# Performance work log

Hardware: AMD Instinct MI355X
Metric: run time of the kernel (lower is better)

## Reference

```python
import jax, jax.numpy as jnp
import numpy as np

HIDDEN = 256
BATCH = 8
N_A = 2048
N_B = 2048


def setup_inputs() -> dict:
    key = jax.random.key(0)
    ks = jax.random.split(key, 9)
    s = 1.0 / np.sqrt(HIDDEN)  # torch Linear default init scale
    return {
        "A": jax.random.normal(ks[0], (BATCH, N_A, HIDDEN), dtype=jnp.float32),
        "B": jax.random.normal(ks[1], (BATCH, N_B, HIDDEN), dtype=jnp.float32),
        "mask_B": jax.random.randint(ks[2], (BATCH, N_B), 0, 2, dtype=jnp.int32),
        "Wq": jax.random.uniform(ks[3], (HIDDEN, HIDDEN), jnp.float32, -s, s),
        "bq": jax.random.uniform(ks[4], (HIDDEN,), jnp.float32, -s, s),
        "Wk": jax.random.uniform(ks[5], (HIDDEN, HIDDEN), jnp.float32, -s, s),
        "bk": jax.random.uniform(ks[6], (HIDDEN,), jnp.float32, -s, s),
        "Wv": jax.random.uniform(ks[7], (HIDDEN, HIDDEN), jnp.float32, -s, s),
        "bv": jax.random.uniform(ks[8], (HIDDEN,), jnp.float32, -s, s),
    }


def reference(A, B, mask_B, Wq, bq, Wk, bk, Wv, bv):
    # QKV projections (torch Linear: x @ W.T + b)
    Q = A @ Wq.T + bq          # [B, N_A, H]
    K = B @ Wk.T + bk          # [B, N_B, H]
    V = B @ Wv.T + bv          # [B, N_B, H]
    scale = 1.0 / jnp.sqrt(jnp.asarray(Q.shape[-1], Q.dtype))
    scores = jnp.einsum("bnh,bmh->bnm", Q, K) * scale  # [B, N_A, N_B]
    neg_inf = jnp.finfo(scores.dtype).min
    scores = jnp.where(mask_B[:, None, :] == 0, neg_inf, scores)
    attn = jax.nn.softmax(scores, axis=-1)
    out = jnp.einsum("bnm,bmh->bnh", attn, V)          # [B, N_A, H]
    return out
```

## Files before the change

kernel.cpp:

```cpp
#include <hip/hip_runtime.h>


typedef __attribute__((ext_vector_type(8))) __bf16 bf16x8;
typedef __attribute__((ext_vector_type(4))) __bf16 bf16x4;
typedef __attribute__((ext_vector_type(4))) float f32x4;

#if __has_builtin(__builtin_amdgcn_exp2f)
#define EXP2(x) __builtin_amdgcn_exp2f(x)
#else
#define EXP2(x) exp2f(x)
#endif

#define MFMA16(a, b, c) __builtin_amdgcn_mfma_f32_16x16x32_bf16((a), (b), (c), 0, 0, 0)

typedef const __attribute__((address_space(1))) char gas_char;
typedef __attribute__((address_space(3))) char las_char;

static __device__ __forceinline__ void gload16(const void* g, void* l) {
  __builtin_amdgcn_global_load_lds((gas_char*)g, (las_char*)l, 16, 0, 0);
}

static __device__ __forceinline__ bf16x8 pack8(f32x4 a, f32x4 b) {
  bf16x8 r;
  r[0] = (__bf16)a[0]; r[1] = (__bf16)a[1]; r[2] = (__bf16)a[2]; r[3] = (__bf16)a[3];
  r[4] = (__bf16)b[0]; r[5] = (__bf16)b[1]; r[6] = (__bf16)b[2]; r[7] = (__bf16)b[3];
  return r;
}

__global__ __launch_bounds__(256) void wprep_kernel(
    const float* __restrict__ Wq, const float* __restrict__ Wk,
    const float* __restrict__ Wv, const int* __restrict__ mask,
    __bf16* __restrict__ Wb, float* __restrict__ mb) {
  const int bid = blockIdx.x;
  if (bid < 96) {
    int c = bid * 256 + threadIdx.x;
    int w_id = c >> 13;
    int j = c & 8191;
    const float* __restrict__ W = (w_id == 0) ? Wq : (w_id == 1 ? Wk : Wv);
    int n = j >> 5;
    int c5 = j & 31;
    int qtr = c5 >> 3;
    int k8 = (c5 & 7) << 3;
    const float* wp = &W[n * 256 + qtr * 64 + k8];
    f32x4 w0 = *(const f32x4*)wp;
    f32x4 w1 = *(const f32x4*)(wp + 4);
    if (w_id == 0) {
      const float cs = 0.090168440f;
      w0[0] *= cs; w0[1] *= cs; w0[2] *= cs; w0[3] *= cs;
      w1[0] *= cs; w1[1] *= cs; w1[2] *= cs; w1[3] *= cs;
    }
    int kx = k8 ^ ((n & 7) << 3);
    *(bf16x8*)&Wb[(size_t)w_id * 65536 + qtr * 16384 + n * 64 + kx] =
        pack8(w0, w1);
  } else {
    int i = (bid - 96) * 256 + threadIdx.x;
    if (i < 8 * 2048) mb[i] = (mask[i] != 0) ? 0.0f : -1.0e30f;
  }
}

__global__ __launch_bounds__(256, 2) void proj_kernel(
    const float* __restrict__ A, const float* __restrict__ Bm,
    const __bf16* __restrict__ Wb,
    const float* __restrict__ bq, const float* __restrict__ bk,
    const float* __restrict__ bv,
    __bf16* __restrict__ QF, __bf16* __restrict__ KF, __bf16* __restrict__ VF) {
  extern __shared__ char smem[];
  const int pid = blockIdx.x;
  const bool isQ = (pid < 256);
  const int rb = (pid & 255) << 6;
  const float* __restrict__ X = isQ ? A : Bm;
  const int tid = threadIdx.x;
  const int w = tid >> 6, l = tid & 63, lo = l & 15, g = l >> 4;
  const int r0 = rb + w * 16;

  #define STAGEW(srcbase, buf)                                                \
    {                                                                         \
      const char* gw = (srcbase) + w * 1024 + l * 16;                         \
      char* lw = smem + (buf)*32768 + w * 1024;                               \
      gload16(gw, lw);                                                        \
      gload16(gw + 4096, lw + 4096);                                          \
      gload16(gw + 8192, lw + 8192);                                          \
      gload16(gw + 12288, lw + 12288);                                        \
      gload16(gw + 16384, lw + 16384);                                        \
      gload16(gw + 20480, lw + 20480);                                        \
      gload16(gw + 24576, lw + 24576);                                        \
      gload16(gw + 28672, lw + 28672);                                        \
    }

  const char* Wq_ = (const char*)Wb;
  const char* Wk_ = (const char*)(Wb + 65536);
  const char* Wv_ = (const char*)(Wb + 131072);

  if (isQ) {
    STAGEW(Wq_, 0);
  } else {
    STAGEW(Wk_, 0);
  }

  bf16x8 xf[8];
#pragma unroll
  for (int q8 = 0; q8 < 8; ++q8) {
    const float* xp = &X[(r0 + lo) * 256 + q8 * 32 + g * 8];
    xf[q8] = pack8(*(const f32x4*)xp, *(const f32x4*)(xp + 4));
  }
  __syncthreads();

  if (isQ) {
    f32x4 acc[16];
#pragma unroll
    for (int j = 0; j < 16; ++j) acc[j] = (f32x4){0.f, 0.f, 0.f, 0.f};
    for (int qtr = 0; qtr < 4; ++qtr) {
      const int cur = qtr & 1;
      if (qtr < 3) STAGEW(Wq_ + (qtr + 1) * 32768, cur ^ 1);
      const __bf16* Wl = (const __bf16*)(smem + cur * 32768);
#pragma unroll
      for (int ks2 = 0; ks2 < 2; ++ks2) {
        bf16x8 xcur = xf[qtr * 2 + ks2];
#pragma unroll
        for (int nt = 0; nt < 16; ++nt) {
          int n = nt * 16 + lo;
          int kchunk = (ks2 * 4 + g) ^ (n & 7);
          bf16x8 wf = *(const bf16x8*)&Wl[n * 64 + kchunk * 8];
          acc[nt] = MFMA16(xcur, wf, acc[nt]);
        }
      }
      __syncthreads();
    }
    const float cs = 0.090168440f;
    const size_t rgbase = (size_t)(r0 >> 4) << 12;
#pragma unroll
    for (int nt = 0; nt < 16; ++nt) {
      int h = nt * 16 + lo;
      float bb = bq[h] * cs;
      size_t hpart = (size_t)((h >> 5) << 9) + (((h >> 3) & 3) << 7) + (h & 7);
#pragma unroll
      for (int r = 0; r < 4; ++r) {
        int R = r0 + g * 4 + r;
        QF[rgbase + hpart + ((R & 15) << 3)] = (__bf16)(acc[nt][r] + bb);
      }
    }
  } else {
    f32x4 accK[16], accV[16];
#pragma unroll
    for (int j = 0; j < 16; ++j) {
      accK[j] = (f32x4){0.f, 0.f, 0.f, 0.f};
      accV[j] = (f32x4){0.f, 0.f, 0.f, 0.f};
    }
    for (int c = 0; c < 8; ++c) {
      const int cur = c & 1;
      if (c < 7) {
        const int cn = c + 1;
        const char* src = ((cn & 1) ? Wv_ : Wk_) + (cn >> 1) * 32768;
        STAGEW(src, cur ^ 1);
      }
      const __bf16* Wl = (const __bf16*)(smem + cur * 32768);
      const int qtr = c >> 1;
#pragma unroll
      for (int ks2 = 0; ks2 < 2; ++ks2) {
        bf16x8 xcur = xf[qtr * 2 + ks2];
#pragma unroll
        for (int nt = 0; nt < 16; ++nt) {
          int n = nt * 16 + lo;
          int kchunk = (ks2 * 4 + g) ^ (n & 7);
          bf16x8 wf = *(const bf16x8*)&Wl[n * 64 + kchunk * 8];
          if (c & 1) {
            accV[nt] = MFMA16(wf, xcur, accV[nt]);
          } else {
            accK[nt] = MFMA16(xcur, wf, accK[nt]);
          }
        }
      }
      __syncthreads();
    }
    const size_t rgbase = (size_t)(r0 >> 4) << 12;
#pragma unroll
    for (int nt = 0; nt < 16; ++nt) {
      int h = nt * 16 + lo;
      float bb = bk[h];
      size_t hpart = (size_t)((h >> 5) << 9) + (((h >> 3) & 3) << 7) + (h & 7);
#pragma unroll
      for (int r = 0; r < 4; ++r) {
        int R = r0 + g * 4 + r;
        KF[rgbase + hpart + ((R & 15) << 3)] = (__bf16)(accK[nt][r] + bb);
      }
    }
    const int bidx = r0 >> 11;
    const int nb = r0 & 2047;
    __bf16* __restrict__ Vo = VF + (size_t)bidx * 524288;
#pragma unroll
    for (int ht = 0; ht < 16; ++ht)
#pragma unroll
      for (int r = 0; r < 4; ++r) {
        int h = ht * 16 + g * 4 + r;
        int n = nb + lo;
        Vo[((size_t)(n >> 6) << 14) + ((h >> 4) << 10) + (((n >> 3) & 7) << 7) +
           ((h & 15) << 3) + (n & 7)] = (__bf16)(accV[ht][r] + bv[h]);
      }
  }
}

__global__ __launch_bounds__(256, 2) void attn_kernel(
    const __bf16* __restrict__ QF, const __bf16* __restrict__ KF,
    const __bf16* __restrict__ VF, const float* __restrict__ mb,
    __bf16* __restrict__ Opart, float* __restrict__ lpart,
    float* __restrict__ out, int chunk, int direct) {
  extern __shared__ char smem[];
  const int bid = blockIdx.x;
  const int b = bid & 7;
  const int rest = bid >> 3;
  const int qt = rest & 15;
  const int s = rest >> 4;
  const int tid = threadIdx.x;
  const int w = tid >> 6, l = tid & 63, lo = l & 15, g = l >> 4;
  const int q0 = qt * 128 + w * 32;
  const __bf16* __restrict__ Qb = QF + ((size_t)b * 2048 + q0) * 256;
  const __bf16* __restrict__ Kb = KF + (size_t)b * 2048 * 256;
  const __bf16* __restrict__ Vb = VF + (size_t)b * 524288;
  const float* __restrict__ mbb = mb + b * 2048;
  __bf16* Pw = (__bf16*)(smem + 65536) + w * 1280;
  float* mbl = (float*)(smem + 75776);

  bf16x8 qf[2][8];
#pragma unroll
  for (int u = 0; u < 2; ++u)
#pragma unroll
    for (int hs = 0; hs < 8; ++hs)
      qf[u][hs] = *(const bf16x8*)&Qb[u * 4096 + hs * 512 + l * 8];

  f32x4 oacc[2][16];
#pragma unroll
  for (int u = 0; u < 2; ++u)
#pragma unroll
    for (int i = 0; i < 16; ++i) oacc[u][i] = (f32x4){0.f, 0.f, 0.f, 0.f};
  float lsum[2] = {0.f, 0.f};

  const int kv0 = s * chunk;
  const int niter = chunk >> 5;

  #define STAGE_K(kvb, buf)                                                   \
    {                                                                         \
      const char* gk = (const char*)(Kb + (size_t)(kvb) * 256) + w * 4096 +   \
                       l * 16;                                                \
      char* lk = smem + (buf)*16384 + w * 4096;                               \
      gload16(gk, lk);                                                        \
      gload16(gk + 1024, lk + 1024);                                          \
      gload16(gk + 2048, lk + 2048);                                          \
      gload16(gk + 3072, lk + 3072);                                          \
    }
  #define STAGE_V(kvb, buf)                                                   \
    {                                                                         \
      const char* gv = (const char*)(Vb + (((size_t)(kvb) >> 6) << 14) +      \
                                     (((kvb) >> 5) & 1) * 512) +              \
                       w * 8192 + l * 16;                                     \
      char* lv = smem + 32768 + (buf)*16384 + w * 4096;                       \
      gload16(gv, lv);                                                        \
      gload16(gv + 2048, lv + 1024);                                          \
      gload16(gv + 4096, lv + 2048);                                          \
      gload16(gv + 6144, lv + 3072);                                          \
    }

  if (!direct)
    for (int j = tid; j < chunk; j += 256) mbl[j] = mbb[kv0 + j];
  STAGE_K(kv0, 0);
  STAGE_V(kv0, 0);
  __syncthreads();

  for (int it = 0; it < niter; ++it) {
    const int kvb = kv0 + (it << 5);
    const int cur = it & 1;
    const bool pre = (it + 1 < niter);
    if (pre) STAGE_K(kvb + 32, cur ^ 1);
    const char* kbase = smem + cur * 16384;
    const char* vbase = smem + 32768 + cur * 16384;

    f32x4 sacc[2][2];
#pragma unroll
    for (int u = 0; u < 2; ++u)
#pragma unroll
      for (int t = 0; t < 2; ++t) sacc[u][t] = (f32x4){0.f, 0.f, 0.f, 0.f};
    __builtin_amdgcn_s_setprio(1);
#pragma unroll
    for (int t = 0; t < 2; ++t)
#pragma unroll
      for (int hs = 0; hs < 8; ++hs) {
        bf16x8 kf = *(const bf16x8*)(kbase + t * 8192 + hs * 1024 + l * 16);
        sacc[0][t] = MFMA16(kf, qf[0][hs], sacc[0][t]);
        sacc[1][t] = MFMA16(kf, qf[1][hs], sacc[1][t]);
      }
    __builtin_amdgcn_s_setprio(0);

    f32x4 bias4[2];
#pragma unroll
    for (int t = 0; t < 2; ++t) {
      if (direct)
        bias4[t] = *(const f32x4*)&mbb[kvb + t * 16 + g * 4];
      else
        bias4[t] = *(const f32x4*)&mbl[(it << 5) + t * 16 + g * 4];
    }
#pragma unroll
    for (int u = 0; u < 2; ++u)
#pragma unroll
      for (int t = 0; t < 2; ++t) {
        float p0 = EXP2(sacc[u][t][0] + bias4[t][0]);
        float p1 = EXP2(sacc[u][t][1] + bias4[t][1]);
        float p2 = EXP2(sacc[u][t][2] + bias4[t][2]);
        float p3 = EXP2(sacc[u][t][3] + bias4[t][3]);
        lsum[u] += (p0 + p1) + (p2 + p3);
        bf16x4 pk;
        pk[0] = (__bf16)p0; pk[1] = (__bf16)p1;
        pk[2] = (__bf16)p2; pk[3] = (__bf16)p3;
        *(bf16x4*)&Pw[u * 640 + lo * 40 + t * 16 + g * 4] = pk;
      }
    bf16x8 pf[2];
#pragma unroll
    for (int u = 0; u < 2; ++u)
      pf[u] = *(const bf16x8*)&Pw[u * 640 + lo * 40 + g * 8];

    if (direct || !pre) {
      asm volatile("s_waitcnt vmcnt(0)" ::: "memory");
    } else {
      asm volatile("s_waitcnt vmcnt(4)" ::: "memory");
    }
    __builtin_amdgcn_s_barrier();
    __builtin_amdgcn_sched_barrier(0);

    if (pre) STAGE_V(kvb + 32, cur ^ 1);

    __builtin_amdgcn_s_setprio(1);
#pragma unroll
    for (int ht = 0; ht < 16; ++ht) {
      bf16x8 vf = *(const bf16x8*)(vbase + ht * 1024 + l * 16);
      oacc[0][ht] = MFMA16(vf, pf[0], oacc[0][ht]);
      oacc[1][ht] = MFMA16(vf, pf[1], oacc[1][ht]);
    }
    __builtin_amdgcn_s_setprio(0);

    if (direct || !pre) {
      asm volatile("s_waitcnt vmcnt(0)" ::: "memory");
    } else {
      asm volatile("s_waitcnt vmcnt(4)" ::: "memory");
    }
    __builtin_amdgcn_s_barrier();
    __builtin_amdgcn_sched_barrier(0);
  }

#pragma unroll
  for (int u = 0; u < 2; ++u) {
    float ls = lsum[u];
    ls += __shfl_xor(ls, 16);
    ls += __shfl_xor(ls, 32);
    const int q0u = q0 + u * 16;
    if (direct) {
      float inv = 1.0f / ls;
      float* __restrict__ Ob = out + ((size_t)b * 2048 + q0u) * 256;
#pragma unroll
      for (int ht = 0; ht < 16; ++ht) {
        f32x4 v = oacc[u][ht];
        v[0] *= inv; v[1] *= inv; v[2] *= inv; v[3] *= inv;
        *(f32x4*)&Ob[lo * 256 + ht * 16 + g * 4] = v;
      }
    } else {
      const size_t rowbase = (size_t)(s * 8 + b) * 2048 + q0u;
      __bf16* __restrict__ Ob = Opart + rowbase * 256;
#pragma unroll
      for (int ht = 0; ht < 16; ++ht) {
        f32x4 v = oacc[u][ht];
        bf16x4 pk;
        pk[0] = (__bf16)v[0]; pk[1] = (__bf16)v[1];
        pk[2] = (__bf16)v[2]; pk[3] = (__bf16)v[3];
        *(bf16x4*)&Ob[lo * 256 + ht * 16 + g * 4] = pk;
      }
      if (l < 16) lpart[rowbase + lo] = ls;
    }
  }
}

__global__ __launch_bounds__(256) void combine_kernel(
    const __bf16* __restrict__ Opart, const float* __restrict__ lpart,
    float* __restrict__ out, int nsplit) {
  int t = blockIdx.x * 256 + threadIdx.x;
  int row = t >> 6;
  int h4 = (t & 63) << 2;
  f32x4 acc = (f32x4){0.f, 0.f, 0.f, 0.f};
  float denom = 0.f;
  for (int s = 0; s < nsplit; ++s) {
    denom += lpart[s * 16384 + row];
    bf16x4 o = *(const bf16x4*)&Opart[((size_t)s * 16384 + row) * 256 + h4];
    acc[0] += (float)o[0]; acc[1] += (float)o[1];
    acc[2] += (float)o[2]; acc[3] += (float)o[3];
  }
  float inv = 1.0f / denom;
  f32x4 r;
  r[0] = acc[0] * inv; r[1] = acc[1] * inv;
  r[2] = acc[2] * inv; r[3] = acc[3] * inv;
  *(f32x4*)&out[(size_t)row * 256 + h4] = r;
}

extern "C" void kernel_launch(void* const* d_in, const int* in_sizes, int n_in,
                              void* d_out, int out_size, void* d_ws, size_t ws_size,
                              hipStream_t stream) {
  const float* A = (const float*)d_in[0];
  const float* B = (const float*)d_in[1];
  const int* mask = (const int*)d_in[2];
  const float* Wq = (const float*)d_in[3];
  const float* bq = (const float*)d_in[4];
  const float* Wk = (const float*)d_in[5];
  const float* bk = (const float*)d_in[6];
  const float* Wv = (const float*)d_in[7];
  const float* bv = (const float*)d_in[8];

  char* ws = (char*)d_ws;
  __bf16* QF = (__bf16*)(ws);
  __bf16* KF = (__bf16*)(ws + (8ull << 20));
  __bf16* VF = (__bf16*)(ws + (16ull << 20));
  float* mb = (float*)(ws + (24ull << 20));
  float* lpart = (float*)(ws + (24ull << 20) + 0x10000);
  __bf16* Wb = (__bf16*)(ws + (24ull << 20) + 0x90000);
  __bf16* Opart = (__bf16*)(ws + (25ull << 20));

  const size_t base = 25ull << 20;
  const size_t part = 8ull << 20;
  int S;
  if (ws_size >= base + 4 * part) S = 4;
  else if (ws_size >= base + 2 * part) S = 2;
  else if (ws_size >= base + 1 * part) S = 1;
  else S = 0;

  const int PSMEM = 65536;
  (void)hipFuncSetAttribute((const void*)proj_kernel,
                            hipFuncAttributeMaxDynamicSharedMemorySize, PSMEM);
  const int SMEM = 65536 + 4 * 1280 * 2 + 2048;
  (void)hipFuncSetAttribute((const void*)attn_kernel,
                            hipFuncAttributeMaxDynamicSharedMemorySize, SMEM);

  wprep_kernel<<<160, 256, 0, stream>>>(Wq, Wk, Wv, mask, Wb, mb);
  proj_kernel<<<512, 256, PSMEM, stream>>>(A, B, Wb, bq, bk, bv, QF, KF, VF);
  if (S == 0) {
    attn_kernel<<<128, 256, SMEM, stream>>>(QF, KF, VF, mb, nullptr, nullptr,
                                            (float*)d_out, 2048, 1);
  } else {
    attn_kernel<<<128 * S, 256, SMEM, stream>>>(QF, KF, VF, mb, Opart, lpart,
                                                nullptr, 2048 / S, 0);
    combine_kernel<<<4096, 256, 0, stream>>>(Opart, lpart, (float*)d_out, S);
  }
}
```

Before: 84.10 us.

## Switch attention loop to 64-wide KV tiles with single-buffered staged K/V

Each attention iteration now processes 64 keys instead of 32. K and V live in a single 32 KB buffer each rather than two double-buffered halves. The next K tile is loaded during the PV MFMAs and the next V tile during the following QK phase, which halves the number of loop iterations and barriers. The mask bias is now read from global memory instead of being staged in LDS. The trade-off is full vmcnt(0) waits and less overlap, since each load must complete before its single buffer is reused.

```diff
diff --git a/kernel.cpp b/kernel.cpp
--- a/kernel.cpp
+++ b/kernel.cpp
@@ -217,8 +217,7 @@
   const __bf16* __restrict__ Kb = KF + (size_t)b * 2048 * 256;
   const __bf16* __restrict__ Vb = VF + (size_t)b * 524288;
   const float* __restrict__ mbb = mb + b * 2048;
-  __bf16* Pw = (__bf16*)(smem + 65536) + w * 1280;
-  float* mbl = (float*)(smem + 75776);
+  __bf16* Pw = (__bf16*)(smem + 65536) + w * 1152;
 
   bf16x8 qf[2][8];
 #pragma unroll
@@ -235,113 +234,106 @@
   float lsum[2] = {0.f, 0.f};
 
   const int kv0 = s * chunk;
-  const int niter = chunk >> 5;
-
-  #define STAGE_K(kvb, buf)                                                   \
+  const int niter = chunk >> 6;
+
+  #define STAGE_K64(kvb)                                                      \
     {                                                                         \
-      const char* gk = (const char*)(Kb + (size_t)(kvb) * 256) + w * 4096 +   \
+      const char* gk = (const char*)(Kb + (size_t)(kvb) * 256) + w * 8192 +   \
                        l * 16;                                                \
-      char* lk = smem + (buf)*16384 + w * 4096;                               \
+      char* lk = smem + w * 8192;                                             \
       gload16(gk, lk);                                                        \
       gload16(gk + 1024, lk + 1024);                                          \
       gload16(gk + 2048, lk + 2048);                                          \
       gload16(gk + 3072, lk + 3072);                                          \
-    }
-  #define STAGE_V(kvb, buf)                                                   \
+      gload16(gk + 4096, lk + 4096);                                          \
+      gload16(gk + 5120, lk + 5120);                                          \
+      gload16(gk + 6144, lk + 6144);                                          \
+      gload16(gk + 7168, lk + 7168);                                          \
+    }
+  #define STAGE_V64(kvb)                                                      \
     {                                                                         \
-      const char* gv = (const char*)(Vb + (((size_t)(kvb) >> 6) << 14) +      \
-                                     (((kvb) >> 5) & 1) * 512) +              \
+      const char* gv = (const char*)(Vb + (((size_t)(kvb) >> 6) << 14)) +     \
                        w * 8192 + l * 16;                                     \
-      char* lv = smem + 32768 + (buf)*16384 + w * 4096;                       \
+      char* lv = smem + 32768 + w * 8192;                                     \
       gload16(gv, lv);                                                        \
-      gload16(gv + 2048, lv + 1024);                                          \
-      gload16(gv + 4096, lv + 2048);                                          \
-      gload16(gv + 6144, lv + 3072);                                          \
-    }
-
-  if (!direct)
-    for (int j = tid; j < chunk; j += 256) mbl[j] = mbb[kv0 + j];
-  STAGE_K(kv0, 0);
-  STAGE_V(kv0, 0);
+      gload16(gv + 1024, lv + 1024);                                          \
+      gload16(gv + 2048, lv + 2048);                                          \
+      gload16(gv + 3072, lv + 3072);                                          \
+      gload16(gv + 4096, lv + 4096);                                          \
+      gload16(gv + 5120, lv + 5120);                                          \
+      gload16(gv + 6144, lv + 6144);                                          \
+      gload16(gv + 7168, lv + 7168);                                          \
+    }
+
+  STAGE_K64(kv0);
+  STAGE_V64(kv0);
   __syncthreads();
 
   for (int it = 0; it < niter; ++it) {
-    const int kvb = kv0 + (it << 5);
-    const int cur = it & 1;
+    const int kvb = kv0 + (it << 6);
     const bool pre = (it + 1 < niter);
-    if (pre) STAGE_K(kvb + 32, cur ^ 1);
-    const char* kbase = smem + cur * 16384;
-    const char* vbase = smem + 32768 + cur * 16384;
-
-    f32x4 sacc[2][2];
-#pragma unroll
-    for (int u = 0; u < 2; ++u)
-#pragma unroll
-      for (int t = 0; t < 2; ++t) sacc[u][t] = (f32x4){0.f, 0.f, 0.f, 0.f};
-    __builtin_amdgcn_s_setprio(1);
-#pragma unroll
-    for (int t = 0; t < 2; ++t)
-#pragma unroll
-      for (int hs = 0; hs < 8; ++hs) {
-        bf16x8 kf = *(const bf16x8*)(kbase + t * 8192 + hs * 1024 + l * 16);
-        sacc[0][t] = MFMA16(kf, qf[0][hs], sacc[0][t]);
-        sacc[1][t] = MFMA16(kf, qf[1][hs], sacc[1][t]);
-      }
-    __builtin_amdgcn_s_setprio(0);
-
-    f32x4 bias4[2];
-#pragma unroll
-    for (int t = 0; t < 2; ++t) {
-      if (direct)
-        bias4[t] = *(const f32x4*)&mbb[kvb + t * 16 + g * 4];
-      else
-        bias4[t] = *(const f32x4*)&mbl[(it << 5) + t * 16 + g * 4];
-    }
-#pragma unroll
-    for (int u = 0; u < 2; ++u)
-#pragma unroll
-      for (int t = 0; t < 2; ++t) {
-        float p0 = EXP2(sacc[u][t][0] + bias4[t][0]);
-        float p1 = EXP2(sacc[u][t][1] + bias4[t][1]);
-        float p2 = EXP2(sacc[u][t][2] + bias4[t][2]);
-        float p3 = EXP2(sacc[u][t][3] + bias4[t][3]);
-        lsum[u] += (p0 + p1) + (p2 + p3);
-        bf16x4 pk;
-        pk[0] = (__bf16)p0; pk[1] = (__bf16)p1;
-        pk[2] = (__bf16)p2; pk[3] = (__bf16)p3;
-        *(bf16x4*)&Pw[u * 640 + lo * 40 + t * 16 + g * 4] = pk;
-      }
-    bf16x8 pf[2];
-#pragma unroll
-    for (int u = 0; u < 2; ++u)
-      pf[u] = *(const bf16x8*)&Pw[u * 640 + lo * 40 + g * 8];
-
-    if (direct || !pre) {
-      asm volatile("s_waitcnt vmcnt(0)" ::: "memory");
-    } else {
-      asm volatile("s_waitcnt vmcnt(4)" ::: "memory");
-    }
+
+    bf16x8 pf[2][2];
+#pragma unroll
+    for (int u = 0; u < 2; ++u) {
+#pragma unroll
+      for (int th = 0; th < 2; ++th) {
+        f32x4 s2[2];
+        s2[0] = (f32x4){0.f, 0.f, 0.f, 0.f};
+        s2[1] = (f32x4){0.f, 0.f, 0.f, 0.f};
+        __builtin_amdgcn_s_setprio(1);
+#pragma unroll
+        for (int t2 = 0; t2 < 2; ++t2) {
+          const int t = th * 2 + t2;
+#pragma unroll
+          for (int hs = 0; hs < 8; ++hs) {
+            bf16x8 kf = *(const bf16x8*)(smem + t * 8192 + hs * 1024 + l * 16);
+            s2[t2] = MFMA16(kf, qf[u][hs], s2[t2]);
+          }
+        }
+        __builtin_amdgcn_s_setprio(0);
+#pragma unroll
+        for (int t2 = 0; t2 < 2; ++t2) {
+          const int t = th * 2 + t2;
+          f32x4 bias4 = *(const f32x4*)&mbb[kvb + t * 16 + g * 4];
+          float p0 = EXP2(s2[t2][0] + bias4[0]);
+          float p1 = EXP2(s2[t2][1] + bias4[1]);
+          float p2 = EXP2(s2[t2][2] + bias4[2]);
+          float p3 = EXP2(s2[t2][3] + bias4[3]);
+          lsum[u] += (p0 + p1) + (p2 + p3);
+          bf16x4 pk;
+          pk[0] = (__bf16)p0; pk[1] = (__bf16)p1;
+          pk[2] = (__bf16)p2; pk[3] = (__bf16)p3;
+          *(bf16x4*)&Pw[lo * 72 + t * 16 + g * 4] = pk;
+        }
+      }
+      pf[u][0] = *(const bf16x8*)&Pw[lo * 72 + g * 8];
+      pf[u][1] = *(const bf16x8*)&Pw[lo * 72 + 32 + g * 8];
+    }
+
+    asm volatile("s_waitcnt vmcnt(0)" ::: "memory");
     __builtin_amdgcn_s_barrier();
     __builtin_amdgcn_sched_barrier(0);
 
-    if (pre) STAGE_V(kvb + 32, cur ^ 1);
+    if (pre) STAGE_K64(kvb + 64);
 
     __builtin_amdgcn_s_setprio(1);
 #pragma unroll
     for (int ht = 0; ht < 16; ++ht) {
-      bf16x8 vf = *(const bf16x8*)(vbase + ht * 1024 + l * 16);
-      oacc[0][ht] = MFMA16(vf, pf[0], oacc[0][ht]);
-      oacc[1][ht] = MFMA16(vf, pf[1], oacc[1][ht]);
+      bf16x8 vf0 = *(const bf16x8*)(smem + 32768 + ht * 2048 + l * 16);
+      bf16x8 vf1 = *(const bf16x8*)(smem + 32768 + ht * 2048 + 1024 + l * 16);
+      oacc[0][ht] = MFMA16(vf0, pf[0][0], oacc[0][ht]);
+      oacc[0][ht] = MFMA16(vf1, pf[0][1], oacc[0][ht]);
+      oacc[1][ht] = MFMA16(vf0, pf[1][0], oacc[1][ht]);
+      oacc[1][ht] = MFMA16(vf1, pf[1][1], oacc[1][ht]);
     }
     __builtin_amdgcn_s_setprio(0);
 
-    if (direct || !pre) {
-      asm volatile("s_waitcnt vmcnt(0)" ::: "memory");
-    } else {
-      asm volatile("s_waitcnt vmcnt(4)" ::: "memory");
-    }
+    asm volatile("s_waitcnt vmcnt(0)" ::: "memory");
     __builtin_amdgcn_s_barrier();
     __builtin_amdgcn_sched_barrier(0);
+
+    if (pre) STAGE_V64(kvb + 64);
   }
 
 #pragma unroll
@@ -429,7 +421,7 @@
   const int PSMEM = 65536;
   (void)hipFuncSetAttribute((const void*)proj_kernel,
                             hipFuncAttributeMaxDynamicSharedMemorySize, PSMEM);
-  const int SMEM = 65536 + 4 * 1280 * 2 + 2048;
+  const int SMEM = 65536 + 4 * 1152 * 2;
   (void)hipFuncSetAttribute((const void*)attn_kernel,
                             hipFuncAttributeMaxDynamicSharedMemorySize, SMEM);
 
```

Result: slower. 94.64 us (+12.5%).
